# Optimization experiments

Hardware: AMD Instinct MI355X
Metric: run time of the kernel (lower is better)

Reference implementation:

```python
import jax, jax.numpy as jnp
import numpy as np
from jax import lax

B, N, D = 4, 64, 32  # graphs, nodes/graph, volume side
HC = 1024            # hidden_channels
NF = 2048            # num_node_features = 32*(D//8)**3
NC = 4               # num_classes
LC = 256             # linear_channels = N*(HC//4)//64


def setup_inputs() -> dict:
    key = jax.random.key(0)
    ks = jax.random.split(key, 16)
    x = jax.random.normal(ks[0], (B, N, D, D, D), jnp.float32)
    # binary symmetric adjacency, zero diagonal (edge presence only; GCNConv ignores values)
    u = jax.random.uniform(ks[1], (B, N, N))
    a = (u < 0.2).astype(jnp.int32)
    a = jnp.maximum(a, a.transpose(0, 2, 1)) * (1 - jnp.eye(N, dtype=jnp.int32))
    s = 0.05
    inp = dict(
        x=x, adj=a, batch_size=B,
        w_conv1=jax.random.normal(ks[2], (16, 1, 3, 3, 3), jnp.float32) * s,
        b_conv1=jnp.zeros((16,), jnp.float32),
        w_conv2=jax.random.normal(ks[3], (32, 16, 3, 3, 3), jnp.float32) * s,
        b_conv2=jnp.zeros((32,), jnp.float32),
        w_g1=jax.random.normal(ks[4], (NF, HC), jnp.float32) * s,
        b_g1=jnp.zeros((HC,), jnp.float32),
        w_g2=jax.random.normal(ks[5], (HC, HC // 2), jnp.float32) * s,
        b_g2=jnp.zeros((HC // 2,), jnp.float32),
        w_g3=jax.random.normal(ks[6], (HC // 2, HC // 4), jnp.float32) * s,
        b_g3=jnp.zeros((HC // 4,), jnp.float32),
        w_fc1=jax.random.normal(ks[7], (LC, 2 * LC), jnp.float32) * s,
        b_fc1=jnp.zeros((2 * LC,), jnp.float32),
        w_fc2=jax.random.normal(ks[8], (2 * LC, NC), jnp.float32) * s,
        b_fc2=jnp.zeros((NC,), jnp.float32),
    )
    return inp


DN = ('NCDHW', 'OIDHW', 'NCDHW')


def _maxpool3(h):
    # MaxPool3d(kernel=3, stride=2, padding=1); pad value -inf matches torch
    return lax.reduce_window(h, -jnp.inf, lax.max,
                             (1, 1, 3, 3, 3), (1, 1, 2, 2, 2),
                             [(0, 0), (0, 0), (1, 1), (1, 1), (1, 1)])


def _gcn_norm(adj, dtype):
    # GCNConv: A_hat = A + I, sym-normalized D^-1/2 A_hat D^-1/2 (per graph)
    A = (adj != 0).astype(dtype) + jnp.eye(adj.shape[-1], dtype=dtype)[None]
    deg = A.sum(-1)                        # [B, N], >= 1
    dinv = deg ** -0.5
    return A * dinv[:, :, None] * dinv[:, None, :]


def _forward(x, adj, batch_size, w_conv1, b_conv1, w_conv2, b_conv2,
             w_g1, b_g1, w_g2, b_g2, w_g3, b_g3, w_fc1, b_fc1, w_fc2, b_fc2):
    b, n = x.shape[0], x.shape[1]
    v = x.reshape(b * n, 1, x.shape[2], x.shape[3], x.shape[4])
    h = lax.conv_general_dilated(v, w_conv1, (1, 1, 1), [(1, 1)] * 3, dimension_numbers=DN)
    h = jax.nn.relu(h + b_conv1[None, :, None, None, None])
    h = _maxpool3(h)                                     # [BN,16,16,16,16]
    h = lax.conv_general_dilated(h, w_conv2, (2, 2, 2), [(1, 1)] * 3, dimension_numbers=DN)
    h = jax.nn.relu(h + b_conv2[None, :, None, None, None])
    h = _maxpool3(h)                                     # [BN,32,4,4,4]
    feat = h.reshape(b, n, -1)                           # [B,N,2048]

    A_norm = _gcn_norm(adj, feat.dtype)                  # [B,N,N]
    gcn = lambda X, W, bb: jnp.einsum('bij,bjf->bif', A_norm, X @ W) + bb
    g = jax.nn.relu(gcn(feat, w_g1, b_g1))
    g = jax.nn.relu(gcn(g, w_g2, b_g2))
    g = gcn(g, w_g3, b_g3)                               # [B,N,256] (no relu, matches source)

    g = g.reshape(batch_size, -1)                        # [B, 16384]
    g = g.reshape(batch_size, -1, 64).max(-1)            # MaxPool1d(64) on 2D input -> [B,256]
    g = jax.nn.relu(g @ w_fc1 + b_fc1)
    return jax.nn.softmax(g @ w_fc2 + b_fc2, axis=-1)


def reference(x, adj, batch_size, w_conv1, b_conv1, w_conv2, b_conv2,
              w_g1, b_g1, w_g2, b_g2, w_g3, b_g3, w_fc1, b_fc1, w_fc2, b_fc2):
    return _forward(x, adj, batch_size, w_conv1, b_conv1, w_conv2, b_conv2,
                    w_g1, b_g1, w_g2, b_g2, w_g3, b_g3, w_fc1, b_fc1, w_fc2, b_fc2)
```

## Files before the change

kernel.cpp:

```cpp
#include <hip/hip_runtime.h>

typedef unsigned short ushort_t;
typedef unsigned long long ull_t;
typedef __attribute__((ext_vector_type(8))) short bf16x8;
typedef __attribute__((ext_vector_type(4))) float f32x4;

static __device__ __forceinline__ unsigned short f2bf(float f) {
  unsigned u = __float_as_uint(f);
  u = (u + 0x7FFFu + ((u >> 16) & 1u)) >> 16;
  return (unsigned short)u;
}

static __device__ __forceinline__ f32x4 max4(f32x4 a, f32x4 b) {
  f32x4 r;
  r[0] = fmaxf(a[0], b[0]); r[1] = fmaxf(a[1], b[1]);
  r[2] = fmaxf(a[2], b[2]); r[3] = fmaxf(a[3], b[3]);
  return r;
}

static __device__ __forceinline__ void gbar(int* bar, int nb) {
  __syncthreads();
  if (threadIdx.x == 0) {
    const int g = atomicAdd(&bar[1], 0);
    __threadfence();
    if (atomicAdd(&bar[0], 1) == nb - 1) {
      atomicExch(&bar[0], 0);
      __threadfence();
      atomicAdd(&bar[1], 1);
    } else {
      for (int it = 0; it < (1 << 24); ++it) {
        if (atomicAdd(&bar[1], 0) != g) break;
        __builtin_amdgcn_s_sleep(8);
      }
    }
    __threadfence();
  }
  __syncthreads();
}


__device__ __forceinline__ void prep_transpose(
    const float* __restrict__ W, ushort_t* __restrict__ out,
    int K, int N, int n0, int k0, int t, float (*tile)[33])
{
  const int tx = t & 31, ty = t >> 5;
#pragma unroll
  for (int i = 0; i < 4; ++i) {
    const int k = k0 + ty + i * 8;
    tile[ty + i * 8][tx] = W[(size_t)k * N + n0 + tx];
  }
  __syncthreads();
#pragma unroll
  for (int i = 0; i < 4; ++i) {
    const int n = n0 + ty + i * 8;
    out[(size_t)n * K + k0 + tx] = f2bf(tile[tx][ty + i * 8]);
  }
}

__global__ __launch_bounds__(256) void k_prep(
    const float* __restrict__ x, ushort_t* __restrict__ xb16,
    const float* __restrict__ w2, ushort_t* __restrict__ w2f,
    const float* __restrict__ wg1, ushort_t* __restrict__ wg1T,
    const float* __restrict__ wg2, ushort_t* __restrict__ wg2T,
    const float* __restrict__ wg3, ushort_t* __restrict__ wg3T,
    const int* __restrict__ adj, float* __restrict__ An)
{
  __shared__ float tile[32][33];
  __shared__ float dinv[64];
  __shared__ int part[256];
  int b = blockIdx.x;
  const int t = threadIdx.x;
  if (b < 8192) {
    const int tid = b * 256 + t;
    const float4 v = ((const float4*)x)[tid];
    const unsigned lo = (unsigned)f2bf(v.x) | ((unsigned)f2bf(v.y) << 16);
    const unsigned hi = (unsigned)f2bf(v.z) | ((unsigned)f2bf(v.w) << 16);
    ((uint2*)xb16)[tid] = make_uint2(lo, hi);
    return;
  }
  b -= 8192;
  if (b < 56) {
    const int tid = b * 256 + t;
    if (tid < 14336) {
      const int nt = tid / 7168, rem = tid % 7168;
      const int kk = rem / 512, rem2 = rem % 512;
      const int l = rem2 >> 3, j = rem2 & 7;
      const int n = nt * 16 + (l & 15);
      const int k = (l >> 4) * 8 + kk * 32 + j;
      float v = 0.f;
      if (k < 432) v = w2[n * 432 + k];
      w2f[tid] = f2bf(v);
    }
    return;
  }
  b -= 56;
  if (b < 2048) { prep_transpose(wg1, wg1T, 2048, 1024, (b & 31) << 5, (b >> 5) << 5, t, tile); return; }
  b -= 2048;
  if (b < 512)  { prep_transpose(wg2, wg2T, 1024, 512,  (b & 15) << 5, (b >> 4) << 5, t, tile); return; }
  b -= 512;
  if (b < 128)  { prep_transpose(wg3, wg3T, 512,  256,  (b & 7)  << 5, (b >> 3) << 5, t, tile); return; }
  b -= 128;
  {
    const int i = t >> 2, q = t & 3;
    const int* ab = adj + b * 4096 + i * 64 + q * 16;
    int d = 0;
#pragma unroll
    for (int j = 0; j < 16; ++j) d += (ab[j] != 0) ? 1 : 0;
    part[t] = d;
    __syncthreads();
    if (q == 0)
      dinv[i] = rsqrtf((float)(1 + part[t] + part[t + 1] + part[t + 2] + part[t + 3]));
    __syncthreads();
    for (int idx = t; idx < 4096; idx += 256) {
      const int ii = idx >> 6, jj = idx & 63;
      const float a = (ii == jj) ? 1.f : ((adj[b * 4096 + idx] != 0) ? 1.f : 0.f);
      An[b * 4096 + idx] = a * dinv[ii] * dinv[jj];
    }
  }
}

__global__ __launch_bounds__(256) void k_conv1_mfma(
    const ushort_t* __restrict__ xb16, const float* __restrict__ wc,
    const float* __restrict__ bc, ushort_t* __restrict__ h1)
{
  __shared__ ushort_t L[2 * 34 * 76];
  char* Lb = (char*)L;
  const int bn = blockIdx.x >> 3, zg = blockIdx.x & 7;
  const int t = threadIdx.x;
  const int w = t >> 6, l = t & 63;
  const int grp = l >> 4, m = l & 15, ch = l & 15;
  const float NINF = -1e30f;

  union { short s[8]; bf16x8 v; } uA, uB;
#pragma unroll
  for (int j = 0; j < 8; ++j) {
    const int k = grp * 8 + j;
    float wA = 0.f, wB = 0.f;
    if (k < 12) {
      const int dx = k >> 2, dz = k & 3;
      if (dz < 3) { wA = wc[ch*27 + dz*9 + 0 + dx]; wB = wc[ch*27 + dz*9 + 6 + dx]; }
    } else if (k >= 16 && k < 28) {
      const int kk = k - 16, dx = kk >> 2, dz = kk & 3;
      if (dz < 3) wA = wc[ch*27 + dz*9 + 3 + dx];
    }
    uA.s[j] = (short)f2bf(wA);
    uB.s[j] = (short)f2bf(wB);
  }

  int aX1[3], aX2[3];
#pragma unroll
  for (int s = 0; s < 3; ++s) {
    const int Q1 = 2*m + s + 2*(grp & 1);
    const int Q2 = Q1 + 1;
    aX1[s] = (Q1 & 1) * 5168 + (Q1 >> 1) * 8;
    aX2[s] = (Q2 & 1) * 5168 + (Q2 >> 1) * 8;
  }
  const int rsel = (grp >> 1) * 152;

  for (int u = t; u < 200; u += 256) {
    int addr;
    if (u < 72) {
      const int rr = (u < 36) ? 0 : 33;
      const int s = (u < 36) ? u : u - 36;
      const int pp = s / 18, slot = s - pp * 18;
      addr = pp * 5168 + rr * 152 + slot * 8;
    } else {
      const int v = u - 72;
      const int rr = 1 + (v >> 2);
      const int pp = (v >> 1) & 1;
      const int slot = (v & 1) * 17;
      addr = pp * 5168 + rr * 152 + slot * 8;
    }
    *(ull_t*)(Lb + addr) = 0ull;
  }

  f32x4 accZ[4][2];
#pragma unroll
  for (int j = 0; j < 4; ++j)
#pragma unroll
    for (int p = 0; p < 2; ++p) accZ[j][p] = (f32x4){NINF, NINF, NINF, NINF};

  const ushort_t* xb = xb16 + (size_t)bn * 32768;

#pragma unroll 1
  for (int ci = 0; ci < 5; ++ci) {
    const int cz = 4*zg - 1 + ci;
    if (cz < 0) continue;
    if (t < 128) {
      const int r = 1 + (t >> 2), g = t & 3;
      const ushort_t* xrow = xb + (r - 1) * 32 + g * 8;
      uint4 u0 = make_uint4(0u, 0u, 0u, 0u), u2 = make_uint4(0u, 0u, 0u, 0u);
      if (cz > 0)  u0 = *(const uint4*)(xrow + (cz - 1) * 1024);
      const uint4 u1 = *(const uint4*)(xrow + cz * 1024);
      if (cz < 31) u2 = *(const uint4*)(xrow + (cz + 1) * 1024);
      char* b0 = Lb + r * 152 + (4 * g + 1) * 8;
      char* b1 = Lb + 5168 + r * 152 + (4 * g + 1) * 8;
      const unsigned* p0 = (const unsigned*)&u0;
      const unsigned* p1 = (const unsigned*)&u1;
      const unsigned* p2 = (const unsigned*)&u2;
#pragma unroll
      for (int e = 0; e < 4; ++e) {
        const unsigned w0 = p0[e], w1 = p1[e], w2v = p2[e];
        const unsigned lo_e = (w0 & 0xFFFFu) | (w1 << 16);
        const unsigned hi_e = (w2v & 0xFFFFu);
        const unsigned lo_o = (w0 >> 16) | (w1 & 0xFFFF0000u);
        const unsigned hi_o = (w2v >> 16);
        *(ull_t*)(b0 + e * 8) = (ull_t)lo_e | ((ull_t)hi_e << 32);
        *(ull_t*)(b1 + e * 8) = (ull_t)lo_o | ((ull_t)hi_o << 32);
      }
    }
    __syncthreads();
    f32x4 accP0 = (f32x4){NINF, NINF, NINF, NINF};
    f32x4 accP1 = (f32x4){NINF, NINF, NINF, NINF};
#pragma unroll
    for (int yy = 0; yy < 9; ++yy) {
      if (yy == 0 && w == 0) continue;
      const int y = 8 * w - 1 + yy;
      const int rbA = y * 152 + rsel;
      const int rbB = (y + 2) * 152;
      f32x4 Cy;
#pragma unroll
      for (int s = 0; s < 3; ++s) {
        union { ull_t u[2]; bf16x8 v; } fA, fB;
        fA.u[0] = *(const ull_t*)(Lb + aX1[s] + rbA);
        fA.u[1] = *(const ull_t*)(Lb + aX2[s] + rbA);
        fB.u[0] = *(const ull_t*)(Lb + aX1[s] + rbB);
        fB.u[1] = *(const ull_t*)(Lb + aX2[s] + rbB);
        f32x4 acc = (f32x4){0.f, 0.f, 0.f, 0.f};
        acc = __builtin_amdgcn_mfma_f32_16x16x32_bf16(fA.v, uA.v, acc, 0, 0, 0);
        acc = __builtin_amdgcn_mfma_f32_16x16x32_bf16(fB.v, uB.v, acc, 0, 0, 0);
        if (s == 0) acc[0] = (l < 16) ? NINF : acc[0];
        Cy = (s == 0) ? acc : max4(Cy, acc);
      }
      if (yy & 1) {
        const int c = (yy - 1) / 2;
        if ((c & 1) == 0) accP0 = max4(accP0, Cy); else accP1 = max4(accP1, Cy);
      } else {
        const int cl = yy / 2 - 1;
        const int chh = yy / 2;
        if (cl >= 0) {
          if ((cl & 1) == 0) {
            accP0 = max4(accP0, Cy);
            if (ci <= 2) accZ[cl][0] = max4(accZ[cl][0], accP0);
            if (ci >= 2) accZ[cl][1] = max4(accZ[cl][1], accP0);
            accP0 = (f32x4){NINF, NINF, NINF, NINF};
          } else {
            accP1 = max4(accP1, Cy);
            if (ci <= 2) accZ[cl][0] = max4(accZ[cl][0], accP1);
            if (ci >= 2) accZ[cl][1] = max4(accZ[cl][1], accP1);
            accP1 = (f32x4){NINF, NINF, NINF, NINF};
          }
        }
        if (chh <= 3) {
          if ((chh & 1) == 0) accP0 = max4(accP0, Cy); else accP1 = max4(accP1, Cy);
        }
      }
    }
    __syncthreads();
  }

  const float biasv = bc[ch];
#pragma unroll
  for (int j = 0; j < 4; ++j) {
    const int py = 4 * w + j;
#pragma unroll
    for (int p = 0; p < 2; ++p) {
      const int pz = 2 * zg + p;
      const f32x4 v = accZ[j][p];
      const unsigned lo = (unsigned)f2bf(fmaxf(v[0] + biasv, 0.f)) |
                          ((unsigned)f2bf(fmaxf(v[1] + biasv, 0.f)) << 16);
      const unsigned hi = (unsigned)f2bf(fmaxf(v[2] + biasv, 0.f)) |
                          ((unsigned)f2bf(fmaxf(v[3] + biasv, 0.f)) << 16);
      ushort_t* dst = h1 + (((size_t)(bn * 16 + ch) * 16 + pz) << 8) + py * 16 + grp * 4;
      *(uint2*)dst = make_uint2(lo, hi);
    }
  }
}

__global__ __launch_bounds__(128) void k_conv2(
    const ushort_t* __restrict__ h1, const ushort_t* __restrict__ w2f,
    float* __restrict__ c2)
{
  __shared__ ushort_t U[16 * 456];
  ushort_t* Hs = U;
  unsigned* Hsd = (unsigned*)U;
  ushort_t* As = U;
  const int b = blockIdx.x;
  const int bn = b >> 5, oz = (b >> 2) & 7, yg = b & 3;
  const int t = threadIdx.x;
  const ushort_t* hb = h1 + ((size_t)bn << 16);
  const int w = t >> 6, l = t & 63;

  bf16x8 bfr[14];
#pragma unroll
  for (int kk = 0; kk < 14; ++kk)
    bfr[kk] = *(const bf16x8*)(const void*)&w2f[(((w * 14) + kk) * 64 + l) * 8];

#pragma unroll
  for (int it = 0; it < 9; ++it) {
    const int u = t + it * 128;
    const int row = u >> 2, q = u & 3;
    const int ic = row / 18;
    const int r2 = row - ic * 18;
    const int izp = r2 / 6;
    const int iyp = r2 - izp * 6;
    const int iz = 2 * oz - 1 + izp;
    const int iy = 4 * yg - 1 + iyp;
    uint2 v = make_uint2(0u, 0u);
    if ((unsigned)iz < 16u && (unsigned)iy < 16u)
      v = *(const uint2*)(hb + (ic << 12) + (iz << 8) + (iy << 4) + q * 4);
    *(uint2*)&Hs[row * 20 + q * 4] = v;
  }
  __syncthreads();

  const int m = t >> 3, sub = t & 7;
  const int ox = m & 7;
  const int my = (m >> 3) * 2;
  ushort_t tv[54];
  int j = 0;
#pragma unroll
  for (int ic2 = 0; ic2 < 2; ++ic2) {
    const int ic = sub * 2 + ic2;
#pragma unroll
    for (int dz = 0; dz < 3; ++dz) {
#pragma unroll
      for (int dy = 0; dy < 3; ++dy) {
        const int row = ic * 18 + dz * 6 + my + dy;
        const unsigned* rp = Hsd + row * 10;
        const unsigned d0 = (ox > 0) ? rp[ox - 1] : 0u;
        const unsigned d1 = rp[ox];
        tv[j]     = (ushort_t)(d0 >> 16);
        tv[j + 1] = (ushort_t)(d1 & 0xFFFFu);
        tv[j + 2] = (ushort_t)(d1 >> 16);
        j += 3;
      }
    }
  }
  __syncthreads();

  {
    unsigned* Aw = (unsigned*)As;
    const int wbase = m * 228 + sub * 27;
#pragma unroll
    for (int p = 0; p < 27; ++p)
      Aw[wbase + p] = (unsigned)tv[2 * p] | ((unsigned)tv[2 * p + 1] << 16);
    Aw[(t >> 3) * 228 + 216 + (t & 7)] = 0u;
  }
  __syncthreads();

  f32x4 acc = {0.f, 0.f, 0.f, 0.f};
  const ushort_t* arow = &As[(l & 15) * 456 + ((l >> 4) << 3)];
#pragma unroll
  for (int kk = 0; kk < 14; ++kk) {
    const bf16x8 af = *(const bf16x8*)(const void*)&arow[kk * 32];
    acc = __builtin_amdgcn_mfma_f32_16x16x32_bf16(af, bfr[kk], acc, 0, 0, 0);
  }
  const int n = w * 16 + (l & 15);
  const int m0 = (l >> 4) << 2;
  float* cb = c2 + (((size_t)(bn * 32 + n) * 8) + oz) * 64 + yg * 16 + m0;
  *(float4*)cb = make_float4(acc[0], acc[1], acc[2], acc[3]);
}

__global__ __launch_bounds__(256) void k_pool2(
    const float* __restrict__ c2, const float* __restrict__ bc2,
    ushort_t* __restrict__ featb, int* __restrict__ bar)
{
  if (blockIdx.x == 0 && threadIdx.x == 0) { bar[0] = 0; bar[1] = 0; }
  const int tid = blockIdx.x * 256 + threadIdx.x;
  const int bn = tid >> 9, r = tid & 511;
  const int ch = r >> 4, pz = (r >> 2) & 3, py = r & 3;
  const float* base = c2 + ((size_t)(bn * 32 + ch) << 9);
  float m0 = -1e30f, m1 = -1e30f, m2 = -1e30f, m3 = -1e30f;
#pragma unroll
  for (int dz = 0; dz < 3; ++dz) {
    const int oz = 2 * pz - 1 + dz;
    if ((unsigned)oz >= 8u) continue;
#pragma unroll
    for (int dy = 0; dy < 3; ++dy) {
      const int oy = 2 * py - 1 + dy;
      if ((unsigned)oy >= 8u) continue;
      const float* row = base + (oz << 6) + (oy << 3);
      const float4 a = ((const float4*)row)[0];
      const float4 b = ((const float4*)row)[1];
      m0 = fmaxf(m0, fmaxf(a.x, a.y));
      m1 = fmaxf(m1, fmaxf(a.y, fmaxf(a.z, a.w)));
      m2 = fmaxf(m2, fmaxf(a.w, fmaxf(b.x, b.y)));
      m3 = fmaxf(m3, fmaxf(b.y, fmaxf(b.z, b.w)));
    }
  }
  const float bb = bc2[ch];
  const unsigned lo = (unsigned)f2bf(fmaxf(m0 + bb, 0.f)) |
                      ((unsigned)f2bf(fmaxf(m1 + bb, 0.f)) << 16);
  const unsigned hi = (unsigned)f2bf(fmaxf(m2 + bb, 0.f)) |
                      ((unsigned)f2bf(fmaxf(m3 + bb, 0.f)) << 16);
  *(uint2*)(featb + (size_t)bn * 2048 + r * 4) = make_uint2(lo, hi);
}

__device__ __forceinline__ void gcn_body(
    const ushort_t* __restrict__ Xb, const ushort_t* __restrict__ WT,
    const float* __restrict__ bias, const float* __restrict__ An,
    ushort_t* __restrict__ Ob, float* __restrict__ spw,
    int K, int N, int relu, int b, int jb,
    ushort_t (*As)[64 * 72], ushort_t (*Bs)[64 * 72], ushort_t* Ps)
{
  const int t = threadIdx.x, w = t >> 6, l = t & 63;
  const int r0 = t >> 3, kc0 = t & 7;
  const int lm = l & 15, lg = l >> 4;

  union { short s[8]; bf16x8 v; } afr[2];
  {
    const float* ap = An + b * 4096 + (16 * w + lm) * 64 + (lg << 3);
#pragma unroll
    for (int kc = 0; kc < 2; ++kc) {
      const float4 v0 = *(const float4*)(ap + kc * 32);
      const float4 v1 = *(const float4*)(ap + kc * 32 + 4);
      afr[kc].s[0] = (short)f2bf(v0.x); afr[kc].s[1] = (short)f2bf(v0.y);
      afr[kc].s[2] = (short)f2bf(v0.z); afr[kc].s[3] = (short)f2bf(v0.w);
      afr[kc].s[4] = (short)f2bf(v1.x); afr[kc].s[5] = (short)f2bf(v1.y);
      afr[kc].s[6] = (short)f2bf(v1.z); afr[kc].s[7] = (short)f2bf(v1.w);
    }
  }

  f32x4 acc[4];
#pragma unroll
  for (int nt = 0; nt < 4; ++nt) acc[nt] = (f32x4){0.f, 0.f, 0.f, 0.f};

  const ushort_t* arow0 = &Xb[(size_t)(b * 64 + r0) * K + kc0 * 8];
  const ushort_t* arow1 = &Xb[(size_t)(b * 64 + r0 + 32) * K + kc0 * 8];
  const ushort_t* brow0 = &WT[(size_t)(jb + r0) * K + kc0 * 8];
  const ushort_t* brow1 = &WT[(size_t)(jb + r0 + 32) * K + kc0 * 8];

  uint4 va0 = *(const uint4*)arow0;
  uint4 va1 = *(const uint4*)arow1;
  uint4 vb0 = *(const uint4*)brow0;
  uint4 vb1 = *(const uint4*)brow1;

  int buf = 0;
#pragma unroll 1
  for (int kt = 0; kt < K; kt += 64) {
    *(uint4*)&As[buf][r0 * 72 + kc0 * 8]        = va0;
    *(uint4*)&As[buf][(r0 + 32) * 72 + kc0 * 8] = va1;
    *(uint4*)&Bs[buf][r0 * 72 + kc0 * 8]        = vb0;
    *(uint4*)&Bs[buf][(r0 + 32) * 72 + kc0 * 8] = vb1;
    __syncthreads();
    if (kt + 64 < K) {
      va0 = *(const uint4*)(arow0 + kt + 64);
      va1 = *(const uint4*)(arow1 + kt + 64);
      vb0 = *(const uint4*)(brow0 + kt + 64);
      vb1 = *(const uint4*)(brow1 + kt + 64);
    }
#pragma unroll
    for (int ks = 0; ks < 2; ++ks) {
      const bf16x8 af = *(const bf16x8*)(const void*)
          &As[buf][(16 * w + lm) * 72 + ks * 32 + (lg << 3)];
#pragma unroll
      for (int nt = 0; nt < 4; ++nt) {
        const bf16x8 bf = *(const bf16x8*)(const void*)
            &Bs[buf][(nt * 16 + lm) * 72 + ks * 32 + (lg << 3)];
        acc[nt] = __builtin_amdgcn_mfma_f32_16x16x32_bf16(af, bf, acc[nt], 0, 0, 0);
      }
    }
    buf ^= 1;
  }

  __syncthreads();
  const int m0 = lg << 2;
#pragma unroll
  for (int nt = 0; nt < 4; ++nt) {
    const int n = nt * 16 + lm;
    const unsigned lo = (unsigned)f2bf(acc[nt][0]) | ((unsigned)f2bf(acc[nt][1]) << 16);
    const unsigned hi = (unsigned)f2bf(acc[nt][2]) | ((unsigned)f2bf(acc[nt][3]) << 16);
    *(uint2*)&Ps[n * 72 + 16 * w + m0] = make_uint2(lo, hi);
  }
  __syncthreads();

  float mx0 = -1e30f, mx1 = -1e30f, mx2 = -1e30f, mx3 = -1e30f;
#pragma unroll
  for (int nt = 0; nt < 4; ++nt) {
    const bf16x8 b0 = *(const bf16x8*)(const void*)&Ps[(nt * 16 + lm) * 72 + (lg << 3)];
    const bf16x8 b1 = *(const bf16x8*)(const void*)&Ps[(nt * 16 + lm) * 72 + 32 + (lg << 3)];
    f32x4 a2 = (f32x4){0.f, 0.f, 0.f, 0.f};
    a2 = __builtin_amdgcn_mfma_f32_16x16x32_bf16(afr[0].v, b0, a2, 0, 0, 0);
    a2 = __builtin_amdgcn_mfma_f32_16x16x32_bf16(afr[1].v, b1, a2, 0, 0, 0);
    const int col = jb + nt * 16 + lm;
    const float bv = bias[col];
    if (spw) {
      mx0 = fmaxf(mx0, a2[0] + bv);
      mx1 = fmaxf(mx1, a2[1] + bv);
      mx2 = fmaxf(mx2, a2[2] + bv);
      mx3 = fmaxf(mx3, a2[3] + bv);
    } else {
#pragma unroll
      for (int r = 0; r < 4; ++r) {
        const int row = b * 64 + 16 * w + m0 + r;
        float v = a2[r] + bv;
        if (relu) v = fmaxf(v, 0.f);
        Ob[(size_t)row * N + col] = f2bf(v);
      }
    }
  }
  if (spw) {
#pragma unroll
    for (int mk = 1; mk <= 8; mk <<= 1) {
      mx0 = fmaxf(mx0, __shfl_xor(mx0, mk));
      mx1 = fmaxf(mx1, __shfl_xor(mx1, mk));
      mx2 = fmaxf(mx2, __shfl_xor(mx2, mk));
      mx3 = fmaxf(mx3, __shfl_xor(mx3, mk));
    }
    if (lm == 0) {
      const int c = jb >> 6;
      const int n = 16 * w + m0;
      spw[b * 256 + (n + 0) * 4 + c] = mx0;
      spw[b * 256 + (n + 1) * 4 + c] = mx1;
      spw[b * 256 + (n + 2) * 4 + c] = mx2;
      spw[b * 256 + (n + 3) * 4 + c] = mx3;
    }
  }
}

__global__ __launch_bounds__(256) void k_tail(
    const ushort_t* __restrict__ featb,
    const ushort_t* __restrict__ wg1T, const float* __restrict__ bg1,
    const ushort_t* __restrict__ wg2T, const float* __restrict__ bg2,
    const ushort_t* __restrict__ wg3T, const float* __restrict__ bg3,
    const float* __restrict__ An,
    ushort_t* __restrict__ g1b, ushort_t* __restrict__ g2b,
    float* __restrict__ spw, float* __restrict__ shw,
    const float* __restrict__ w1, const float* __restrict__ b1,
    const float* __restrict__ w2, const float* __restrict__ b2,
    float* __restrict__ out, int* __restrict__ bar)
{
  __shared__ ushort_t As[2][64 * 72];
  __shared__ ushort_t Bs[2][64 * 72];
  __shared__ ushort_t Ps[64 * 72];
  __shared__ float red[260];
  const int bx = blockIdx.x, t = threadIdx.x;

  gcn_body(featb, wg1T, bg1, An, g1b, nullptr, 2048, 1024, 1,
           bx >> 4, (bx & 15) << 6, As, Bs, Ps);
  gbar(bar, 64);

  if (bx < 32)
    gcn_body(g1b, wg2T, bg2, An, g2b, nullptr, 1024, 512, 1,
             bx >> 3, (bx & 7) << 6, As, Bs, Ps);
  gbar(bar, 64);

  if (bx < 16)
    gcn_body(g2b, wg3T, bg3, An, nullptr, spw, 512, 256, 0,
             bx >> 2, (bx & 3) << 6, As, Bs, Ps);
  gbar(bar, 64);

  {
    const int oo = t & 31, ks = t >> 5;
    const int bb = bx >> 4;
    const int jj = (bx & 15) * 32 + oo;
    const float* spb = spw + bb * 256;
    float s = 0.f;
#pragma unroll
    for (int i = 0; i < 32; ++i) {
      const int k = ks * 32 + i;
      s += spb[k] * w1[k * 512 + jj];
    }
    red[t] = s;
    __syncthreads();
    if (t < 32) {
      float s2 = 0.f;
#pragma unroll
      for (int i = 0; i < 8; ++i) s2 += red[t + i * 32];
      const int j2 = (bx & 15) * 32 + t;
      shw[bb * 512 + j2] = fmaxf(s2 + b1[j2], 0.f);
    }
  }
  gbar(bar, 64);

  if (bx < 4) {
    float s = 0.f;
    if (t < 128) {
      const int c = t & 3, ks2 = t >> 2;
      const float* shb = shw + bx * 512;
#pragma unroll
      for (int i = 0; i < 16; ++i) {
        const int k = ks2 * 16 + i;
        s += shb[k] * w2[k * 4 + c];
      }
    }
    red[t] = s;
    __syncthreads();
    if (t < 4) {
      float s2 = b2[t];
#pragma unroll
      for (int i = 0; i < 32; ++i) s2 += red[t + i * 4];
      red[256 + t] = s2;
    }
    __syncthreads();
    if (t == 0) {
      const float a0 = red[256], a1 = red[257], a2v = red[258], a3 = red[259];
      const float mm = fmaxf(fmaxf(a0, a1), fmaxf(a2v, a3));
      const float e0 = expf(a0 - mm), e1 = expf(a1 - mm);
      const float e2 = expf(a2v - mm), e3 = expf(a3 - mm);
      const float inv = 1.f / (e0 + e1 + e2 + e3);
      out[bx * 4 + 0] = e0 * inv;
      out[bx * 4 + 1] = e1 * inv;
      out[bx * 4 + 2] = e2 * inv;
      out[bx * 4 + 3] = e3 * inv;
    }
  }
}

extern "C" void kernel_launch(void* const* d_in, const int* in_sizes, int n_in,
                              void* d_out, int out_size, void* d_ws, size_t ws_size,
                              hipStream_t stream)
{
  (void)in_sizes; (void)n_in; (void)out_size; (void)ws_size;
  const float* x   = (const float*)d_in[0];
  const int*   adj = (const int*)d_in[1];
  const float* wc1 = (const float*)d_in[3];
  const float* bc1 = (const float*)d_in[4];
  const float* wc2 = (const float*)d_in[5];
  const float* bc2 = (const float*)d_in[6];
  const float* wg1 = (const float*)d_in[7];
  const float* bg1 = (const float*)d_in[8];
  const float* wg2 = (const float*)d_in[9];
  const float* bg2 = (const float*)d_in[10];
  const float* wg3 = (const float*)d_in[11];
  const float* bg3 = (const float*)d_in[12];
  const float* wf1 = (const float*)d_in[13];
  const float* bf1 = (const float*)d_in[14];
  const float* wf2 = (const float*)d_in[15];
  const float* bf2 = (const float*)d_in[16];

  float* ws    = (float*)d_ws;
  ushort_t* h1 = (ushort_t*)d_ws;
  ushort_t* w2f   = (ushort_t*)(ws + 8388608);
  ushort_t* wg1Tb = (ushort_t*)(ws + 8395776);
  ushort_t* wg2Tb = (ushort_t*)(ws + 9444352);
  ushort_t* wg3Tb = (ushort_t*)(ws + 9706496);
  ushort_t* featb = (ushort_t*)(ws + 9772032);
  ushort_t* g1b   = (ushort_t*)(ws + 10034176);
  ushort_t* g2b   = (ushort_t*)(ws + 10165248);
  float* c2    = ws + 16777216;
  ushort_t* xb16 = (ushort_t*)(ws + 16777216);
  float* An   = ws + 21495808;
  float* spw  = ws + 10034176;
  float* shw  = ws + 10035200;
  int*   bar  = (int*)(ws + 22364160);
  float* outp = (float*)d_out;

  hipLaunchKernelGGL(k_prep,        dim3(10940),    dim3(256), 0, stream,
                     x, xb16, wc2, w2f, wg1, wg1Tb, wg2, wg2Tb, wg3, wg3Tb, adj, An);
  hipLaunchKernelGGL(k_conv1_mfma,  dim3(2048),     dim3(256), 0, stream, xb16, wc1, bc1, h1);
  hipLaunchKernelGGL(k_conv2,       dim3(8192),     dim3(128), 0, stream, h1, w2f, c2);
  hipLaunchKernelGGL(k_pool2,       dim3(512),      dim3(256), 0, stream, c2, bc2, featb, bar);
  hipLaunchKernelGGL(k_tail,        dim3(64),       dim3(256), 0, stream,
                     featb, wg1Tb, bg1, wg2Tb, bg2, wg3Tb, bg3, An, g1b, g2b,
                     spw, shw, wf1, bf1, wf2, bf2, outp, bar);
}
```

Baseline: 249.9 us.

## Split-K the GCN XW GEMMs across 256 blocks with fp32 partial reduction

The tail kernel now runs 256 blocks instead of 64. Each GCN layer's X@W product is split along K into partial fp32 tiles written to workspace, and a separate phase sums those partials and applies the normalized adjacency, bias and ReLU. The aim is to use more compute units for the weight-bandwidth-bound GEMMs. In exchange there are extra grid barriers, more blocks to synchronise, and partial-sum traffic through global memory. The threadfence in the barrier is also moved ahead of the block sync.

```diff
diff --git a/kernel.cpp b/kernel.cpp
--- a/kernel.cpp
+++ b/kernel.cpp
@@ -19,10 +19,10 @@
 }
 
 static __device__ __forceinline__ void gbar(int* bar, int nb) {
+  __threadfence();
   __syncthreads();
   if (threadIdx.x == 0) {
     const int g = atomicAdd(&bar[1], 0);
-    __threadfence();
     if (atomicAdd(&bar[0], 1) == nb - 1) {
       atomicExch(&bar[0], 0);
       __threadfence();
@@ -396,15 +396,72 @@
   *(uint2*)(featb + (size_t)bn * 2048 + r * 4) = make_uint2(lo, hi);
 }
 
-__device__ __forceinline__ void gcn_body(
+__device__ __forceinline__ void gemm_xw_partial(
     const ushort_t* __restrict__ Xb, const ushort_t* __restrict__ WT,
-    const float* __restrict__ bias, const float* __restrict__ An,
-    ushort_t* __restrict__ Ob, float* __restrict__ spw,
-    int K, int N, int relu, int b, int jb,
-    ushort_t (*As)[64 * 72], ushort_t (*Bs)[64 * 72], ushort_t* Ps)
+    float* __restrict__ Pout, int Kfull, int KC, int k0, int rows0, int cols0,
+    ushort_t (*As)[64 * 72], ushort_t (*Bs)[64 * 72])
 {
   const int t = threadIdx.x, w = t >> 6, l = t & 63;
   const int r0 = t >> 3, kc0 = t & 7;
+  const int lm = l & 15, lg = l >> 4;
+
+  f32x4 acc[4];
+#pragma unroll
+  for (int nt = 0; nt < 4; ++nt) acc[nt] = (f32x4){0.f, 0.f, 0.f, 0.f};
+
+  const ushort_t* arow0 = &Xb[(size_t)(rows0 + r0) * Kfull + k0 + kc0 * 8];
+  const ushort_t* arow1 = &Xb[(size_t)(rows0 + r0 + 32) * Kfull + k0 + kc0 * 8];
+  const ushort_t* brow0 = &WT[(size_t)(cols0 + r0) * Kfull + k0 + kc0 * 8];
+  const ushort_t* brow1 = &WT[(size_t)(cols0 + r0 + 32) * Kfull + k0 + kc0 * 8];
+
+  uint4 va0 = *(const uint4*)arow0;
+  uint4 va1 = *(const uint4*)arow1;
+  uint4 vb0 = *(const uint4*)brow0;
+  uint4 vb1 = *(const uint4*)brow1;
+
+  int buf = 0;
+#pragma unroll 1
+  for (int kt = 0; kt < KC; kt += 64) {
+    *(uint4*)&As[buf][r0 * 72 + kc0 * 8]        = va0;
+    *(uint4*)&As[buf][(r0 + 32) * 72 + kc0 * 8] = va1;
+    *(uint4*)&Bs[buf][r0 * 72 + kc0 * 8]        = vb0;
+    *(uint4*)&Bs[buf][(r0 + 32) * 72 + kc0 * 8] = vb1;
+    __syncthreads();
+    if (kt + 64 < KC) {
+      va0 = *(const uint4*)(arow0 + kt + 64);
+      va1 = *(const uint4*)(arow1 + kt + 64);
+      vb0 = *(const uint4*)(brow0 + kt + 64);
+      vb1 = *(const uint4*)(brow1 + kt + 64);
+    }
+#pragma unroll
+    for (int ks = 0; ks < 2; ++ks) {
+      const bf16x8 af = *(const bf16x8*)(const void*)
+          &As[buf][(16 * w + lm) * 72 + ks * 32 + (lg << 3)];
+#pragma unroll
+      for (int nt = 0; nt < 4; ++nt) {
+        const bf16x8 bf = *(const bf16x8*)(const void*)
+            &Bs[buf][(nt * 16 + lm) * 72 + ks * 32 + (lg << 3)];
+        acc[nt] = __builtin_amdgcn_mfma_f32_16x16x32_bf16(af, bf, acc[nt], 0, 0, 0);
+      }
+    }
+    buf ^= 1;
+  }
+
+  const int m0 = lg << 2;
+#pragma unroll
+  for (int nt = 0; nt < 4; ++nt)
+#pragma unroll
+    for (int r = 0; r < 4; ++r)
+      Pout[(16 * w + m0 + r) * 64 + nt * 16 + lm] = acc[nt][r];
+}
+
+__device__ __forceinline__ void anp_body(
+    const float* __restrict__ Pp, int nsplit, int ntiles, int tile,
+    const float* __restrict__ An, const float* __restrict__ bias,
+    ushort_t* __restrict__ Ob, float* __restrict__ spw,
+    int N, int relu, int b, int jb, ushort_t* Ps)
+{
+  const int t = threadIdx.x, w = t >> 6, l = t & 63;
   const int lm = l & 15, lg = l >> 4;
 
   union { short s[8]; bf16x8 v; } afr[2];
@@ -421,59 +478,28 @@
     }
   }
 
-  f32x4 acc[4];
-#pragma unroll
-  for (int nt = 0; nt < 4; ++nt) acc[nt] = (f32x4){0.f, 0.f, 0.f, 0.f};
-
-  const ushort_t* arow0 = &Xb[(size_t)(b * 64 + r0) * K + kc0 * 8];
-  const ushort_t* arow1 = &Xb[(size_t)(b * 64 + r0 + 32) * K + kc0 * 8];
-  const ushort_t* brow0 = &WT[(size_t)(jb + r0) * K + kc0 * 8];
-  const ushort_t* brow1 = &WT[(size_t)(jb + r0 + 32) * K + kc0 * 8];
-
-  uint4 va0 = *(const uint4*)arow0;
-  uint4 va1 = *(const uint4*)arow1;
-  uint4 vb0 = *(const uint4*)brow0;
-  uint4 vb1 = *(const uint4*)brow1;
-
-  int buf = 0;
-#pragma unroll 1
-  for (int kt = 0; kt < K; kt += 64) {
-    *(uint4*)&As[buf][r0 * 72 + kc0 * 8]        = va0;
-    *(uint4*)&As[buf][(r0 + 32) * 72 + kc0 * 8] = va1;
-    *(uint4*)&Bs[buf][r0 * 72 + kc0 * 8]        = vb0;
-    *(uint4*)&Bs[buf][(r0 + 32) * 72 + kc0 * 8] = vb1;
-    __syncthreads();
-    if (kt + 64 < K) {
-      va0 = *(const uint4*)(arow0 + kt + 64);
-      va1 = *(const uint4*)(arow1 + kt + 64);
-      vb0 = *(const uint4*)(brow0 + kt + 64);
-      vb1 = *(const uint4*)(brow1 + kt + 64);
-    }
-#pragma unroll
-    for (int ks = 0; ks < 2; ++ks) {
-      const bf16x8 af = *(const bf16x8*)(const void*)
-          &As[buf][(16 * w + lm) * 72 + ks * 32 + (lg << 3)];
-#pragma unroll
-      for (int nt = 0; nt < 4; ++nt) {
-        const bf16x8 bf = *(const bf16x8*)(const void*)
-            &Bs[buf][(nt * 16 + lm) * 72 + ks * 32 + (lg << 3)];
-        acc[nt] = __builtin_amdgcn_mfma_f32_16x16x32_bf16(af, bf, acc[nt], 0, 0, 0);
-      }
-    }
-    buf ^= 1;
-  }
-
+  {
+    const int kq = t >> 2, nq = t & 3;
+    const float* pt = Pp + (size_t)tile * 4096 + kq * 64 + nq * 16;
+    float sv[16];
+#pragma unroll
+    for (int j = 0; j < 16; ++j) sv[j] = 0.f;
+    for (int ks = 0; ks < nsplit; ++ks) {
+      const float* p = pt + (size_t)ks * ntiles * 4096;
+#pragma unroll
+      for (int j4 = 0; j4 < 4; ++j4) {
+        const float4 v = *(const float4*)(p + j4 * 4);
+        sv[j4 * 4 + 0] += v.x; sv[j4 * 4 + 1] += v.y;
+        sv[j4 * 4 + 2] += v.z; sv[j4 * 4 + 3] += v.w;
+      }
+    }
+#pragma unroll
+    for (int j = 0; j < 16; ++j)
+      Ps[(nq * 16 + j) * 72 + kq] = f2bf(sv[j]);
+  }
   __syncthreads();
+
   const int m0 = lg << 2;
-#pragma unroll
-  for (int nt = 0; nt < 4; ++nt) {
-    const int n = nt * 16 + lm;
-    const unsigned lo = (unsigned)f2bf(acc[nt][0]) | ((unsigned)f2bf(acc[nt][1]) << 16);
-    const unsigned hi = (unsigned)f2bf(acc[nt][2]) | ((unsigned)f2bf(acc[nt][3]) << 16);
-    *(uint2*)&Ps[n * 72 + 16 * w + m0] = make_uint2(lo, hi);
-  }
-  __syncthreads();
-
   float mx0 = -1e30f, mx1 = -1e30f, mx2 = -1e30f, mx3 = -1e30f;
 #pragma unroll
   for (int nt = 0; nt < 4; ++nt) {
@@ -523,7 +549,7 @@
     const ushort_t* __restrict__ wg1T, const float* __restrict__ bg1,
     const ushort_t* __restrict__ wg2T, const float* __restrict__ bg2,
     const ushort_t* __restrict__ wg3T, const float* __restrict__ bg3,
-    const float* __restrict__ An,
+    const float* __restrict__ An, float* __restrict__ Pp,
     ushort_t* __restrict__ g1b, ushort_t* __restrict__ g2b,
     float* __restrict__ spw, float* __restrict__ shw,
     const float* __restrict__ w1, const float* __restrict__ b1,
@@ -535,22 +561,47 @@
   __shared__ ushort_t Ps[64 * 72];
   __shared__ float red[260];
   const int bx = blockIdx.x, t = threadIdx.x;
-
-  gcn_body(featb, wg1T, bg1, An, g1b, nullptr, 2048, 1024, 1,
-           bx >> 4, (bx & 15) << 6, As, Bs, Ps);
-  gbar(bar, 64);
+  float* Pp1 = Pp;
+  float* Pp2 = Pp + (1 << 20);
+  float* Pp3 = Pp + (2 << 20);
+
+  {
+    const int ks = bx >> 6, tile = bx & 63;
+    gemm_xw_partial(featb, wg1T, Pp1 + (size_t)bx * 4096, 2048, 512, ks * 512,
+                    (tile >> 4) * 64, (tile & 15) * 64, As, Bs);
+  }
+  gbar(bar, 256);
+
+  if (bx < 64)
+    anp_body(Pp1, 4, 64, bx, An, bg1, g1b, nullptr, 1024, 1,
+             bx >> 4, (bx & 15) << 6, Ps);
+  gbar(bar, 256);
+
+  {
+    const int ks = bx >> 5, tile = bx & 31;
+    gemm_xw_partial(g1b, wg2T, Pp2 + (size_t)bx * 4096, 1024, 128, ks * 128,
+                    (tile >> 3) * 64, (tile & 7) * 64, As, Bs);
+  }
+  gbar(bar, 256);
 
   if (bx < 32)
-    gcn_body(g1b, wg2T, bg2, An, g2b, nullptr, 1024, 512, 1,
-             bx >> 3, (bx & 7) << 6, As, Bs, Ps);
-  gbar(bar, 64);
+    anp_body(Pp2, 8, 32, bx, An, bg2, g2b, nullptr, 512, 1,
+             bx >> 3, (bx & 7) << 6, Ps);
+  gbar(bar, 256);
+
+  if (bx < 128) {
+    const int ks = bx >> 4, tile = bx & 15;
+    gemm_xw_partial(g2b, wg3T, Pp3 + (size_t)bx * 4096, 512, 64, ks * 64,
+                    (tile >> 2) * 64, (tile & 3) * 64, As, Bs);
+  }
+  gbar(bar, 256);
 
   if (bx < 16)
-    gcn_body(g2b, wg3T, bg3, An, nullptr, spw, 512, 256, 0,
-             bx >> 2, (bx & 3) << 6, As, Bs, Ps);
-  gbar(bar, 64);
-
-  {
+    anp_body(Pp3, 8, 16, bx, An, bg3, nullptr, spw, 256, 0,
+             bx >> 2, (bx & 3) << 6, Ps);
+  gbar(bar, 256);
+
+  if (bx < 64) {
     const int oo = t & 31, ks = t >> 5;
     const int bb = bx >> 4;
     const int jj = (bx & 15) * 32 + oo;
@@ -571,7 +622,7 @@
       shw[bb * 512 + j2] = fmaxf(s2 + b1[j2], 0.f);
     }
   }
-  gbar(bar, 64);
+  gbar(bar, 256);
 
   if (bx < 4) {
     float s = 0.f;
@@ -641,8 +692,9 @@
   float* c2    = ws + 16777216;
   ushort_t* xb16 = (ushort_t*)(ws + 16777216);
   float* An   = ws + 21495808;
-  float* spw  = ws + 10034176;
-  float* shw  = ws + 10035200;
+  float* Pp   = ws;
+  float* spw  = ws + 2621440;
+  float* shw  = ws + 2622464;
   int*   bar  = (int*)(ws + 22364160);
   float* outp = (float*)d_out;
 
@@ -651,7 +703,7 @@
   hipLaunchKernelGGL(k_conv1_mfma,  dim3(2048),     dim3(256), 0, stream, xb16, wc1, bc1, h1);
   hipLaunchKernelGGL(k_conv2,       dim3(8192),     dim3(128), 0, stream, h1, w2f, c2);
   hipLaunchKernelGGL(k_pool2,       dim3(512),      dim3(256), 0, stream, c2, bc2, featb, bar);
-  hipLaunchKernelGGL(k_tail,        dim3(64),       dim3(256), 0, stream,
-                     featb, wg1Tb, bg1, wg2Tb, bg2, wg3Tb, bg3, An, g1b, g2b,
+  hipLaunchKernelGGL(k_tail,        dim3(256),      dim3(256), 0, stream,
+                     featb, wg1Tb, bg1, wg2Tb, bg2, wg3Tb, bg3, An, Pp, g1b, g2b,
                      spw, shw, wf1, bf1, wf2, bf2, outp, bar);
 }
```

New measurement: 491.4 us. 1.97x slower.

## Use hierarchical grid barrier and fold fc1 into final blocks to drop a barrier

Applied to the files above, without the earlier changes.

Replaces the flat atomic grid barrier with a two-level tree barrier (8 leaf counters, then a root) that uses scoped acquire/release atomics and mostly relaxed polling with shorter sleeps. This cuts contention on a single counter. The fc1 layer is no longer spread over all 64 blocks with a barrier afterwards. Instead the 4 per-graph blocks each compute the full 256x512 matvec from shared memory, which removes one grid barrier and the round trip through global memory for the hidden vector, at the cost of more serial work per block. The spw scratch buffer is also moved to a different workspace offset.

```diff
diff --git a/kernel.cpp b/kernel.cpp
--- a/kernel.cpp
+++ b/kernel.cpp
@@ -19,18 +19,38 @@
 }
 
 static __device__ __forceinline__ void gbar(int* bar, int nb) {
+  __threadfence();
   __syncthreads();
   if (threadIdx.x == 0) {
-    const int g = atomicAdd(&bar[1], 0);
-    __threadfence();
-    if (atomicAdd(&bar[0], 1) == nb - 1) {
-      atomicExch(&bar[0], 0);
-      __threadfence();
-      atomicAdd(&bar[1], 1);
-    } else {
-      for (int it = 0; it < (1 << 24); ++it) {
-        if (atomicAdd(&bar[1], 0) != g) break;
-        __builtin_amdgcn_s_sleep(8);
+    const int g = __hip_atomic_load(&bar[320], __ATOMIC_RELAXED,
+                                    __HIP_MEMORY_SCOPE_AGENT);
+    const int leaf = (blockIdx.x & 7) << 5;
+    const int nl = nb >> 3;
+    bool final_block = false;
+    if (__hip_atomic_fetch_add(&bar[leaf], 1, __ATOMIC_ACQ_REL,
+                               __HIP_MEMORY_SCOPE_AGENT) == nl - 1) {
+      __hip_atomic_store(&bar[leaf], 0, __ATOMIC_RELAXED,
+                         __HIP_MEMORY_SCOPE_AGENT);
+      if (__hip_atomic_fetch_add(&bar[256], 1, __ATOMIC_ACQ_REL,
+                                 __HIP_MEMORY_SCOPE_AGENT) == 7) {
+        __hip_atomic_store(&bar[256], 0, __ATOMIC_RELAXED,
+                           __HIP_MEMORY_SCOPE_AGENT);
+        __hip_atomic_fetch_add(&bar[320], 1, __ATOMIC_RELEASE,
+                               __HIP_MEMORY_SCOPE_AGENT);
+        final_block = true;
+      }
+    }
+    if (!final_block) {
+      for (int it = 0; it < (1 << 20); ++it) {
+        int cur;
+        if ((it & 63) == 63)
+          cur = __hip_atomic_fetch_add(&bar[320], 0, __ATOMIC_ACQUIRE,
+                                       __HIP_MEMORY_SCOPE_AGENT);
+        else
+          cur = __hip_atomic_load(&bar[320], __ATOMIC_RELAXED,
+                                  __HIP_MEMORY_SCOPE_AGENT);
+        if (cur != g) break;
+        __builtin_amdgcn_s_sleep(4);
       }
     }
     __threadfence();
@@ -365,7 +385,9 @@
     const float* __restrict__ c2, const float* __restrict__ bc2,
     ushort_t* __restrict__ featb, int* __restrict__ bar)
 {
-  if (blockIdx.x == 0 && threadIdx.x == 0) { bar[0] = 0; bar[1] = 0; }
+  if (blockIdx.x == 0) {
+    for (int i = threadIdx.x; i < 384; i += 256) bar[i] = 0;
+  }
   const int tid = blockIdx.x * 256 + threadIdx.x;
   const int bn = tid >> 9, r = tid & 511;
   const int ch = r >> 4, pz = (r >> 2) & 3, py = r & 3;
@@ -525,7 +547,7 @@
     const ushort_t* __restrict__ wg3T, const float* __restrict__ bg3,
     const float* __restrict__ An,
     ushort_t* __restrict__ g1b, ushort_t* __restrict__ g2b,
-    float* __restrict__ spw, float* __restrict__ shw,
+    float* __restrict__ spw,
     const float* __restrict__ w1, const float* __restrict__ b1,
     const float* __restrict__ w2, const float* __restrict__ b2,
     float* __restrict__ out, int* __restrict__ bar)
@@ -534,6 +556,8 @@
   __shared__ ushort_t Bs[2][64 * 72];
   __shared__ ushort_t Ps[64 * 72];
   __shared__ float red[260];
+  __shared__ float sp[256];
+  __shared__ float sh[512];
   const int bx = blockIdx.x, t = threadIdx.x;
 
   gcn_body(featb, wg1T, bg1, An, g1b, nullptr, 2048, 1024, 1,
@@ -550,38 +574,26 @@
              bx >> 2, (bx & 3) << 6, As, Bs, Ps);
   gbar(bar, 64);
 
-  {
-    const int oo = t & 31, ks = t >> 5;
-    const int bb = bx >> 4;
-    const int jj = (bx & 15) * 32 + oo;
-    const float* spb = spw + bb * 256;
-    float s = 0.f;
-#pragma unroll
-    for (int i = 0; i < 32; ++i) {
-      const int k = ks * 32 + i;
-      s += spb[k] * w1[k * 512 + jj];
-    }
-    red[t] = s;
-    __syncthreads();
-    if (t < 32) {
-      float s2 = 0.f;
-#pragma unroll
-      for (int i = 0; i < 8; ++i) s2 += red[t + i * 32];
-      const int j2 = (bx & 15) * 32 + t;
-      shw[bb * 512 + j2] = fmaxf(s2 + b1[j2], 0.f);
-    }
-  }
-  gbar(bar, 64);
-
   if (bx < 4) {
+    sp[t] = spw[bx * 256 + t];
+    __syncthreads();
+    float s0 = b1[t], s1 = b1[t + 256];
+#pragma unroll 4
+    for (int k = 0; k < 256; ++k) {
+      const float xv = sp[k];
+      s0 += xv * w1[k * 512 + t];
+      s1 += xv * w1[k * 512 + t + 256];
+    }
+    sh[t] = fmaxf(s0, 0.f);
+    sh[t + 256] = fmaxf(s1, 0.f);
+    __syncthreads();
     float s = 0.f;
     if (t < 128) {
       const int c = t & 3, ks2 = t >> 2;
-      const float* shb = shw + bx * 512;
 #pragma unroll
       for (int i = 0; i < 16; ++i) {
         const int k = ks2 * 16 + i;
-        s += shb[k] * w2[k * 4 + c];
+        s += sh[k] * w2[k * 4 + c];
       }
     }
     red[t] = s;
@@ -641,8 +653,7 @@
   float* c2    = ws + 16777216;
   ushort_t* xb16 = (ushort_t*)(ws + 16777216);
   float* An   = ws + 21495808;
-  float* spw  = ws + 10034176;
-  float* shw  = ws + 10035200;
+  float* spw  = ws + 2621440;
   int*   bar  = (int*)(ws + 22364160);
   float* outp = (float*)d_out;
 
@@ -653,5 +664,5 @@
   hipLaunchKernelGGL(k_pool2,       dim3(512),      dim3(256), 0, stream, c2, bc2, featb, bar);
   hipLaunchKernelGGL(k_tail,        dim3(64),       dim3(256), 0, stream,
                      featb, wg1Tb, bg1, wg2Tb, bg2, wg3Tb, bg3, An, g1b, g2b,
-                     spw, shw, wf1, bf1, wf2, bf2, outp, bar);
-}
+                     spw, wf1, bf1, wf2, bf2, outp, bar);
+}
```

New measurement: 280.5 us. 1.12x slower.
